# Performance work log

Hardware: AMD Instinct MI355X
Metric: run time of the kernel (lower is better)

Reference implementation:

```python
import jax, jax.numpy as jnp
import numpy as np
from jax import lax

K_NEIGHBORS = 128  # args.k_neighbors


def setup_inputs() -> dict:
    key = jax.random.key(0)
    k1, k2, k3 = jax.random.split(key, 3)
    images = jax.random.normal(k1, (16, 3, 32, 32), dtype=jnp.float32)
    # patch dictionary: [n_patches=2048, C_in=3, p=6, p=6]
    kernel = jax.random.normal(k2, (2048, 3, 6, 6), dtype=jnp.float32)
    # bias = squared patch norms / 2 (positive), shape [n_patches]
    bias = jax.random.uniform(k3, (2048,), dtype=jnp.float32)
    return {"images": images, "kernel": kernel, "bias": bias}


def _conv(images, kernel):
    # NCHW x OIHW -> NCHW, VALID conv (matches F.conv2d with no padding/stride)
    return lax.conv_general_dilated(
        images, kernel, window_strides=(1, 1), padding='VALID',
        dimension_numbers=('NCHW', 'OIHW', 'NCHW'))


def reference(images, kernel, bias):
    conv = _conv(images, kernel)                       # [B, P, H', W']
    # hflip of kernel = flip along last (width) axis
    conv_flip = _conv(images, kernel[..., ::-1])       # [B, P, H', W']
    b = bias[None, :, None, None]                      # [1, P, 1, 1]
    # order matches torch: [pos, flipped_pos, neg, flipped_neg]
    d = jnp.concatenate([-conv + b, -conv_flip + b, conv + b, conv_flip + b],
                        axis=1)                        # [B, 4P, H', W']
    # torch kthvalue(k=K+1, dim=1) -> (K+1)-th smallest = 0-indexed K after partition
    kth = jnp.partition(d, K_NEIGHBORS, axis=1)[:, K_NEIGHBORS:K_NEIGHBORS + 1]
    return jnp.where(d < kth, jnp.float32(1.0), jnp.float32(0.0))
```

## Files before the change

kernel.cpp:

```cpp
#include <hip/hip_runtime.h>


#define NPOS 729
#define NTHR 11664
#define FCH 16

__device__ __forceinline__ unsigned map32(float x) {
    unsigned v = __float_as_uint(x);
    return (v & 0x80000000u) ? ~v : (v | 0x80000000u);
}

__global__ __launch_bounds__(128) void prep_w1(
    const float* __restrict__ wgt, float* __restrict__ s1)
{
    int f = blockIdx.x;
    int t = threadIdx.x;
    s1[f * 128 + t] = (t < 108) ? wgt[f * 108 + t] : 0.f;
}

#define RLW(pos) __int_as_float(__builtin_amdgcn_readlane(                      \
    ((pos) < 64 ? wv0 : wv1), (pos) & 63))
#define WIDX(ci, kh, kw) (((ci) * 6 + (kh)) * 6 + (kw))

__global__ __launch_bounds__(256) void conv_rl34(
    const float* __restrict__ img, const float* __restrict__ s1,
    float2* __restrict__ B3, float2* __restrict__ B4)
{
    int bx = blockIdx.x;
    int fg = bx & 127;
    int rest = bx >> 7;
    int pg = rest % 3;
    int n  = rest / 3;
    int t  = threadIdx.x;
    int lane = t & 63;

    bool act = t < 243;
    int p  = pg * 243 + (act ? t : 242);
    int oh = p / 27, ow = p % 27;

    float x[3][6][6];
    #pragma unroll
    for (int ci = 0; ci < 3; ci++)
        #pragma unroll
        for (int kh = 0; kh < 6; kh++)
            #pragma unroll
            for (int kw = 0; kw < 6; kw++)
                x[ci][kh][kw] = img[((n * 3 + ci) * 32 + oh + kh) * 32 + ow + kw];

    const int* sw = (const int*)s1;
    int f0 = fg * FCH;
    int wv0 = sw[f0 * 128 + lane];
    int wv1 = sw[f0 * 128 + 64 + lane];

    #pragma unroll 1
    for (int fi = 0; fi < FCH; fi++) {
        int f = f0 + fi;
        int nf = (fi == FCH - 1) ? f : (f + 1);
        int nv0 = sw[nf * 128 + lane];
        int nv1 = sw[nf * 128 + 64 + lane];

        float c3 = 0.f, cf3 = 0.f, c4 = 0.f, cf4 = 0.f;

        #pragma unroll
        for (int kh = 0; kh < 6; kh++)
            #pragma unroll
            for (int kw = 0; kw < 6; kw++)
                #pragma unroll
                for (int ci = 0; ci < 3; ci++) {
                    float wa = RLW(WIDX(ci, kh, kw));
                    float wb = RLW(WIDX(ci, kh, 5 - kw));
                    float xx = x[ci][kh][kw];
                    c3  = __fadd_rn(c3,  __fmul_rn(wa, xx));
                    cf3 = __fadd_rn(cf3, __fmul_rn(wb, xx));
                }

        #pragma unroll
        for (int kw = 0; kw < 6; kw++)
            #pragma unroll
            for (int kh = 0; kh < 6; kh++)
                #pragma unroll
                for (int ci = 0; ci < 3; ci++) {
                    float wa = RLW(WIDX(ci, kh, kw));
                    float wb = RLW(WIDX(ci, kh, 5 - kw));
                    float xx = x[ci][kh][kw];
                    c4  = fmaf(wa, xx, c4);
                    cf4 = fmaf(wb, xx, cf4);
                }

        if (act) {
            B3[((long)n * 2048 + f) * NPOS + p] = make_float2(c3, cf3);
            B4[((long)n * 2048 + f) * NPOS + p] = make_float2(c4, cf4);
        }
        wv0 = nv0; wv1 = nv1;
    }
}

__global__ __launch_bounds__(64) void thresh34(
    const float2* __restrict__ B3, const float2* __restrict__ B4,
    const float* __restrict__ bias, unsigned* __restrict__ thr)
{
    int bx = blockIdx.x;
    int w  = (bx & 7) * 1458 + (bx >> 3);
    int n = w / NPOS;
    int p = w % NPOS;
    int lane = threadIdx.x;

    unsigned m3[64], m4[64];
    #pragma unroll
    for (int j = 0; j < 32; j++) {
        int f = lane + 64 * j;
        float2 v3 = B3[((long)n * 2048 + f) * NPOS + p];
        float2 v4 = B4[((long)n * 2048 + f) * NPOS + p];
        float b = bias[f];
        m3[2*j]   = min(map32(__fsub_rn(b, v3.x)), map32(__fadd_rn(v3.x, b)));
        m3[2*j+1] = min(map32(__fsub_rn(b, v3.y)), map32(__fadd_rn(v3.y, b)));
        m4[2*j]   = min(map32(__fsub_rn(b, v4.x)), map32(__fadd_rn(v4.x, b)));
        m4[2*j+1] = min(map32(__fsub_rn(b, v4.y)), map32(__fadd_rn(v4.y, b)));
    }

    unsigned P3 = 0, P4 = 0;
    #pragma unroll 1
    for (int bit = 31; bit >= 0; bit--) {
        unsigned C3 = P3 | (1u << bit);
        unsigned C4 = P4 | (1u << bit);
        int cnt = 0;
        #pragma unroll
        for (int j = 0; j < 64; j++) {
            cnt += (m3[j] < C3) ? 1 : 0;
            cnt += (m4[j] < C4) ? (1 << 16) : 0;
        }
        #pragma unroll
        for (int off = 32; off >= 1; off >>= 1) cnt += __shfl_xor(cnt, off, 64);
        if ((cnt & 0xFFFF) <= 128) P3 = C3;
        if ((cnt >> 16)    <= 128) P4 = C4;
    }
    if (lane == 0) {
        thr[n * NPOS + p]        = P3;
        thr[NTHR + n * NPOS + p] = P4;
    }
}

__global__ __launch_bounds__(256) void writeout(
    const float2* __restrict__ B3, const float2* __restrict__ B4,
    const float* __restrict__ bias, const unsigned* __restrict__ thr,
    float* __restrict__ out)
{
    int bx = blockIdx.x;
    int grp = bx % 3;
    int rest = bx / 3;
    int ftile = rest & 31;
    int n = rest >> 5;
    int t = threadIdx.x;
    int w = t >> 6, lane = t & 63;
    int p = (grp * 4 + w) * 64 + lane;
    bool act = p < NPOS;

    unsigned P3 = 0, P4 = 0;
    if (act) {
        P3 = thr[n * NPOS + p];
        P4 = thr[NTHR + n * NPOS + p];
    }
    long nb = (long)n * 8192 * NPOS;

    #pragma unroll 1
    for (int fi = 0; fi < 64; fi++) {
        int f = ftile * 64 + fi;
        float b = bias[f];
        if (act) {
            float2 v3 = B3[((long)n * 2048 + f) * NPOS + p];
            float2 v4 = B4[((long)n * 2048 + f) * NPOS + p];
            int s0 = (map32(__fsub_rn(b, v3.x)) < P3) && (map32(__fsub_rn(b, v4.x)) < P4);
            int s1 = (map32(__fsub_rn(b, v3.y)) < P3) && (map32(__fsub_rn(b, v4.y)) < P4);
            int s2 = (map32(__fadd_rn(v3.x, b)) < P3) && (map32(__fadd_rn(v4.x, b)) < P4);
            int s3 = (map32(__fadd_rn(v3.y, b)) < P3) && (map32(__fadd_rn(v4.y, b)) < P4);
            out[nb + (long)(f       ) * NPOS + p] = s0 ? 1.0f : 0.0f;
            out[nb + (long)(f + 2048) * NPOS + p] = s1 ? 1.0f : 0.0f;
            out[nb + (long)(f + 4096) * NPOS + p] = s2 ? 1.0f : 0.0f;
            out[nb + (long)(f + 6144) * NPOS + p] = s3 ? 1.0f : 0.0f;
        }
    }
}

__global__ __launch_bounds__(256) void conv_h34(
    const float* __restrict__ img, const float* __restrict__ wgt,
    float* __restrict__ out)
{
    int bx = blockIdx.x;
    int ftile = bx & 31;
    int rest  = bx >> 5;
    int oh = rest % 27;
    int n  = rest / 27;
    int t  = threadIdx.x;

    __shared__ float wl[64][109];
    __shared__ float patch[3][6][32];
    for (int idx = t; idx < 64 * 108; idx += 256) {
        int fi = idx / 108, k = idx - fi * 108;
        wl[fi][k] = wgt[(ftile * 64 + fi) * 108 + k];
    }
    for (int idx = t; idx < 576; idx += 256) {
        int w = idx & 31, rr = idx >> 5;
        int ci = rr / 6, r = rr - ci * 6;
        patch[ci][r][w] = img[((n * 3 + ci) * 32 + (oh + r)) * 32 + w];
    }
    __syncthreads();

    int fidx = t & 63;
    int g    = t >> 6;
    int ow0  = g * 7;
    int ncols = (g < 3) ? 7 : 6;
    int f = ftile * 64 + fidx;
    long nb = (long)n * 8192 * NPOS;
    long pb = (long)oh * 27;

    #pragma unroll 1
    for (int i = 0; i < ncols; i++) {
        int ow = ow0 + i;
        float c3 = 0, cf3 = 0, c4 = 0, cf4 = 0;
        #pragma unroll
        for (int kh = 0; kh < 6; kh++)
        #pragma unroll
        for (int kw = 0; kw < 6; kw++)
        #pragma unroll
        for (int ci = 0; ci < 3; ci++) {
            float x = patch[ci][kh][ow + kw];
            c3  = __fadd_rn(c3,  __fmul_rn(wl[fidx][(ci*6+kh)*6 + kw],     x));
            cf3 = __fadd_rn(cf3, __fmul_rn(wl[fidx][(ci*6+kh)*6 + 5 - kw], x));
        }
        #pragma unroll
        for (int kw = 0; kw < 6; kw++)
        #pragma unroll
        for (int kh = 0; kh < 6; kh++)
        #pragma unroll
        for (int ci = 0; ci < 3; ci++) {
            float x = patch[ci][kh][ow + kw];
            c4  = fmaf(wl[fidx][(ci*6+kh)*6 + kw],     x, c4);
            cf4 = fmaf(wl[fidx][(ci*6+kh)*6 + 5 - kw], x, cf4);
        }
        long pp = pb + ow;
        out[nb + (long)(f       ) * NPOS + pp] = c3;
        out[nb + (long)(f + 2048) * NPOS + pp] = cf3;
        out[nb + (long)(f + 4096) * NPOS + pp] = c4;
        out[nb + (long)(f + 6144) * NPOS + pp] = cf4;
    }
}

__device__ __forceinline__ unsigned bisect128(const unsigned (&u)[4][8],
                                              int lane, int wid, int* partial)
{
    unsigned P = 0;
    #pragma unroll 1
    for (int bit = 31; bit >= 0; bit--) {
        unsigned C = P | (1u << bit);
        int cnt = 0;
        #pragma unroll
        for (int q = 0; q < 4; q++)
            #pragma unroll
            for (int j = 0; j < 8; j++) cnt += (u[q][j] < C) ? 1 : 0;
        #pragma unroll
        for (int off = 32; off >= 1; off >>= 1) cnt += __shfl_xor(cnt, off, 64);
        if (lane == 0) partial[wid] = cnt;
        __syncthreads();
        int tot = partial[0] + partial[1] + partial[2] + partial[3];
        __syncthreads();
        if (tot <= 128) P = C;
    }
    return P;
}

__global__ __launch_bounds__(256) void sel_h34(
    const float* __restrict__ bias, float* out)
{
    int bx = blockIdx.x;
    int n = bx / NPOS;
    int p = bx % NPOS;
    int t = threadIdx.x;
    int lane = t & 63, wid = t >> 6;
    __shared__ int partial[4];

    unsigned u3[4][8], u4[4][8];
    long nb = (long)n * 8192 * NPOS;
    #pragma unroll
    for (int j = 0; j < 8; j++) {
        int f = t + 256 * j;
        float c3  = out[nb + (long)(f       ) * NPOS + p];
        float cf3 = out[nb + (long)(f + 2048) * NPOS + p];
        float c4  = out[nb + (long)(f + 4096) * NPOS + p];
        float cf4 = out[nb + (long)(f + 6144) * NPOS + p];
        float b   = bias[f];
        u3[0][j] = map32(__fsub_rn(b, c3));
        u3[1][j] = map32(__fsub_rn(b, cf3));
        u3[2][j] = map32(__fadd_rn(c3, b));
        u3[3][j] = map32(__fadd_rn(cf3, b));
        u4[0][j] = map32(__fsub_rn(b, c4));
        u4[1][j] = map32(__fsub_rn(b, cf4));
        u4[2][j] = map32(__fadd_rn(c4, b));
        u4[3][j] = map32(__fadd_rn(cf4, b));
    }
    unsigned P3 = bisect128(u3, lane, wid, partial);
    unsigned P4 = bisect128(u4, lane, wid, partial);
    #pragma unroll
    for (int j = 0; j < 8; j++) {
        int f = t + 256 * j;
        #pragma unroll
        for (int q = 0; q < 4; q++) {
            int s = (u3[q][j] < P3) && (u4[q][j] < P4);
            out[nb + (long)(q * 2048 + f) * NPOS + p] = s ? 1.0f : 0.0f;
        }
    }
}

extern "C" void kernel_launch(void* const* d_in, const int* in_sizes, int n_in,
                              void* d_out, int out_size, void* d_ws, size_t ws_size,
                              hipStream_t stream)
{
    const float* img  = (const float*)d_in[0];
    const float* wgt  = (const float*)d_in[1];
    const float* bias = (const float*)d_in[2];
    float* out = (float*)d_out;

    size_t halfB = (size_t)16 * 2048 * NPOS * sizeof(float2);
    size_t thrB  = (size_t)2 * NTHR * sizeof(unsigned);
    size_t s1B   = (size_t)2048 * 128 * sizeof(float);
    size_t need  = 2 * halfB + thrB + s1B;

    if (ws_size >= need) {
        float2*   B3  = (float2*)d_ws;
        float2*   B4  = (float2*)((char*)d_ws + halfB);
        unsigned* thr = (unsigned*)((char*)d_ws + 2 * halfB);
        float*    s1  = (float*)((char*)d_ws + 2 * halfB + thrB);
        prep_w1<<<2048, 128, 0, stream>>>(wgt, s1);
        conv_rl34<<<128 * 3 * 16, 256, 0, stream>>>(img, s1, B3, B4);
        thresh34<<<NTHR, 64, 0, stream>>>(B3, B4, bias, thr);
        writeout<<<16 * 32 * 3, 256, 0, stream>>>(B3, B4, bias, thr, out);
    } else {
        conv_h34<<<16 * 27 * 32, 256, 0, stream>>>(img, wgt, out);
        sel_h34<<<NTHR, 256, 0, stream>>>(bias, out);
    }
}
```

Baseline: 958.6 us.

## Interleave conv buffers into float4 and widen threshold search to 256 threads

The two float2 intermediate buffers are merged into one interleaved float4 buffer, so each (image, filter, position) entry is read with a single 16-byte load in the threshold and writeout kernels. The radix-select threshold kernel now uses 256 threads per position instead of 64. Each thread holds far fewer values in registers, and wave partial counts are combined through double-buffered shared memory with one barrier per bit. This aims to cut register pressure and raise occupancy in the threshold kernel, at the cost of 32 block-level synchronizations per position.

```diff
diff --git a/kernel.cpp b/kernel.cpp
--- a/kernel.cpp
+++ b/kernel.cpp
@@ -24,7 +24,7 @@
 
 __global__ __launch_bounds__(256) void conv_rl34(
     const float* __restrict__ img, const float* __restrict__ s1,
-    float2* __restrict__ B3, float2* __restrict__ B4)
+    float4* __restrict__ Bp)
 {
     int bx = blockIdx.x;
     int fg = bx & 127;
@@ -87,37 +87,36 @@
                     cf4 = fmaf(wb, xx, cf4);
                 }
 
-        if (act) {
-            B3[((long)n * 2048 + f) * NPOS + p] = make_float2(c3, cf3);
-            B4[((long)n * 2048 + f) * NPOS + p] = make_float2(c4, cf4);
-        }
+        if (act)
+            Bp[((long)n * 2048 + f) * NPOS + p] = make_float4(c3, cf3, c4, cf4);
         wv0 = nv0; wv1 = nv1;
     }
 }
 
-__global__ __launch_bounds__(64) void thresh34(
-    const float2* __restrict__ B3, const float2* __restrict__ B4,
-    const float* __restrict__ bias, unsigned* __restrict__ thr)
+__global__ __launch_bounds__(256) void thresh_kernel(
+    const float4* __restrict__ Bp, const float* __restrict__ bias,
+    unsigned* __restrict__ thr)
 {
     int bx = blockIdx.x;
     int w  = (bx & 7) * 1458 + (bx >> 3);
     int n = w / NPOS;
     int p = w % NPOS;
-    int lane = threadIdx.x;
-
-    unsigned m3[64], m4[64];
+    int t = threadIdx.x;
+    int lane = t & 63, wid = t >> 6;
+
+    unsigned m3[2][8], m4[2][8];
     #pragma unroll
-    for (int j = 0; j < 32; j++) {
-        int f = lane + 64 * j;
-        float2 v3 = B3[((long)n * 2048 + f) * NPOS + p];
-        float2 v4 = B4[((long)n * 2048 + f) * NPOS + p];
+    for (int j = 0; j < 8; j++) {
+        int f = t + 256 * j;
+        float4 v = Bp[((long)n * 2048 + f) * NPOS + p];
         float b = bias[f];
-        m3[2*j]   = min(map32(__fsub_rn(b, v3.x)), map32(__fadd_rn(v3.x, b)));
-        m3[2*j+1] = min(map32(__fsub_rn(b, v3.y)), map32(__fadd_rn(v3.y, b)));
-        m4[2*j]   = min(map32(__fsub_rn(b, v4.x)), map32(__fadd_rn(v4.x, b)));
-        m4[2*j+1] = min(map32(__fsub_rn(b, v4.y)), map32(__fadd_rn(v4.y, b)));
-    }
-
+        m3[0][j] = min(map32(__fsub_rn(b, v.x)), map32(__fadd_rn(v.x, b)));
+        m3[1][j] = min(map32(__fsub_rn(b, v.y)), map32(__fadd_rn(v.y, b)));
+        m4[0][j] = min(map32(__fsub_rn(b, v.z)), map32(__fadd_rn(v.z, b)));
+        m4[1][j] = min(map32(__fsub_rn(b, v.w)), map32(__fadd_rn(v.w, b)));
+    }
+
+    __shared__ int partial[2][4];
     unsigned P3 = 0, P4 = 0;
     #pragma unroll 1
     for (int bit = 31; bit >= 0; bit--) {
@@ -125,25 +124,30 @@
         unsigned C4 = P4 | (1u << bit);
         int cnt = 0;
         #pragma unroll
-        for (int j = 0; j < 64; j++) {
-            cnt += (m3[j] < C3) ? 1 : 0;
-            cnt += (m4[j] < C4) ? (1 << 16) : 0;
+        for (int k = 0; k < 2; k++)
+        #pragma unroll
+        for (int j = 0; j < 8; j++) {
+            cnt += (m3[k][j] < C3) ? 1 : 0;
+            cnt += (m4[k][j] < C4) ? (1 << 16) : 0;
         }
         #pragma unroll
         for (int off = 32; off >= 1; off >>= 1) cnt += __shfl_xor(cnt, off, 64);
-        if ((cnt & 0xFFFF) <= 128) P3 = C3;
-        if ((cnt >> 16)    <= 128) P4 = C4;
-    }
-    if (lane == 0) {
+        int par = bit & 1;
+        if (lane == 0) partial[par][wid] = cnt;
+        __syncthreads();
+        int tot = partial[par][0] + partial[par][1] + partial[par][2] + partial[par][3];
+        if ((tot & 0xFFFF) <= 128) P3 = C3;
+        if ((tot >> 16)    <= 128) P4 = C4;
+    }
+    if (t == 0) {
         thr[n * NPOS + p]        = P3;
         thr[NTHR + n * NPOS + p] = P4;
     }
 }
 
 __global__ __launch_bounds__(256) void writeout(
-    const float2* __restrict__ B3, const float2* __restrict__ B4,
-    const float* __restrict__ bias, const unsigned* __restrict__ thr,
-    float* __restrict__ out)
+    const float4* __restrict__ Bp, const float* __restrict__ bias,
+    const unsigned* __restrict__ thr, float* __restrict__ out)
 {
     int bx = blockIdx.x;
     int grp = bx % 3;
@@ -167,12 +171,11 @@
         int f = ftile * 64 + fi;
         float b = bias[f];
         if (act) {
-            float2 v3 = B3[((long)n * 2048 + f) * NPOS + p];
-            float2 v4 = B4[((long)n * 2048 + f) * NPOS + p];
-            int s0 = (map32(__fsub_rn(b, v3.x)) < P3) && (map32(__fsub_rn(b, v4.x)) < P4);
-            int s1 = (map32(__fsub_rn(b, v3.y)) < P3) && (map32(__fsub_rn(b, v4.y)) < P4);
-            int s2 = (map32(__fadd_rn(v3.x, b)) < P3) && (map32(__fadd_rn(v4.x, b)) < P4);
-            int s3 = (map32(__fadd_rn(v3.y, b)) < P3) && (map32(__fadd_rn(v4.y, b)) < P4);
+            float4 v = Bp[((long)n * 2048 + f) * NPOS + p];
+            int s0 = (map32(__fsub_rn(b, v.x)) < P3) && (map32(__fsub_rn(b, v.z)) < P4);
+            int s1 = (map32(__fsub_rn(b, v.y)) < P3) && (map32(__fsub_rn(b, v.w)) < P4);
+            int s2 = (map32(__fadd_rn(v.x, b)) < P3) && (map32(__fadd_rn(v.z, b)) < P4);
+            int s3 = (map32(__fadd_rn(v.y, b)) < P3) && (map32(__fadd_rn(v.w, b)) < P4);
             out[nb + (long)(f       ) * NPOS + p] = s0 ? 1.0f : 0.0f;
             out[nb + (long)(f + 2048) * NPOS + p] = s1 ? 1.0f : 0.0f;
             out[nb + (long)(f + 4096) * NPOS + p] = s2 ? 1.0f : 0.0f;
@@ -319,20 +322,19 @@
     const float* bias = (const float*)d_in[2];
     float* out = (float*)d_out;
 
-    size_t halfB = (size_t)16 * 2048 * NPOS * sizeof(float2);
-    size_t thrB  = (size_t)2 * NTHR * sizeof(unsigned);
-    size_t s1B   = (size_t)2048 * 128 * sizeof(float);
-    size_t need  = 2 * halfB + thrB + s1B;
+    size_t bpB  = (size_t)16 * 2048 * NPOS * sizeof(float4);
+    size_t thrB = (size_t)2 * NTHR * sizeof(unsigned);
+    size_t s1B  = (size_t)2048 * 128 * sizeof(float);
+    size_t need = bpB + thrB + s1B;
 
     if (ws_size >= need) {
-        float2*   B3  = (float2*)d_ws;
-        float2*   B4  = (float2*)((char*)d_ws + halfB);
-        unsigned* thr = (unsigned*)((char*)d_ws + 2 * halfB);
-        float*    s1  = (float*)((char*)d_ws + 2 * halfB + thrB);
+        float4*   Bp  = (float4*)d_ws;
+        unsigned* thr = (unsigned*)((char*)d_ws + bpB);
+        float*    s1  = (float*)((char*)d_ws + bpB + thrB);
         prep_w1<<<2048, 128, 0, stream>>>(wgt, s1);
-        conv_rl34<<<128 * 3 * 16, 256, 0, stream>>>(img, s1, B3, B4);
-        thresh34<<<NTHR, 64, 0, stream>>>(B3, B4, bias, thr);
-        writeout<<<16 * 32 * 3, 256, 0, stream>>>(B3, B4, bias, thr, out);
+        conv_rl34<<<128 * 3 * 16, 256, 0, stream>>>(img, s1, Bp);
+        thresh_kernel<<<NTHR, 256, 0, stream>>>(Bp, bias, thr);
+        writeout<<<16 * 32 * 3, 256, 0, stream>>>(Bp, bias, thr, out);
     } else {
         conv_h34<<<16 * 27 * 32, 256, 0, stream>>>(img, wgt, out);
         sel_h34<<<NTHR, 256, 0, stream>>>(bias, out);
```

Result: faster. 819.5 us (median of 2 runs) (-14.5%).
